# Kernel optimization log

Measured on AMD Instinct MI355X. Metric: run time of the kernel, lower is better.

## Reference

```python
import jax, jax.numpy as jnp
import numpy as np

C = 1024
T = 2048
B = 8

def setup_inputs() -> dict:
    key = jax.random.key(0)
    ks = jax.random.split(key, 7)
    s = lambda fan_in: 1.0 / np.sqrt(fan_in)
    return {
        "x":     jax.random.normal(ks[0], (B, T, C), dtype=jnp.float32),
        "w_qkv": jax.random.uniform(ks[1], (C, 3 * C), jnp.float32, -s(C), s(C)),
        "w_proj": jax.random.uniform(ks[2], (C, C), jnp.float32, -s(C), s(C)),
        "w1":    jax.random.uniform(ks[3], (C, 2 * C), jnp.float32, -s(C), s(C)),
        "w2":    jax.random.uniform(ks[4], (2 * C, C), jnp.float32, -s(2 * C), s(2 * C)),
        "g1":    jnp.ones((C,), jnp.float32),
        "g2":    jnp.ones((C,), jnp.float32),
    }

def rmsnorm(x, g, eps=1e-6):
    return x * jax.lax.rsqrt(jnp.mean(x * x, axis=-1, keepdims=True) + eps) * g

def reference(x, w_qkv, w_proj, w1, w2, g1, g2):
    t = x.shape[1]
    # --- attention ---
    h = rmsnorm(x, g1)
    qkv = h @ w_qkv                               # [B,T,3C]
    q, k, v = jnp.split(qkv, 3, axis=-1)
    scores = jnp.einsum('bqc,bkc->bqk', q, k) * (C ** -0.5)  # [B,T,T]
    causal = jnp.triu(jnp.ones((t, t), dtype=bool), k=1)
    scores = jnp.where(causal, -jnp.inf, scores)
    attn = jax.nn.softmax(scores, axis=-1)
    x = x + (attn @ v) @ w_proj
    # --- ffn ---
    h = rmsnorm(x, g2)
    return x + (jax.nn.silu(h @ w1)) @ w2
```

## Files before the change

### kernel.cpp

```cpp
#include <hip/hip_runtime.h>
#include <hip/hip_bf16.h>
#include <stdint.h>


#define C_DIM 1024
#define T_DIM 2048
#define B_DIM 8

typedef float f32x4 __attribute__((ext_vector_type(4)));
typedef __bf16 bf16x8 __attribute__((ext_vector_type(8)));

typedef const __attribute__((address_space(1))) void gvoid_t;
typedef __attribute__((address_space(3))) void lvoid_t;

__device__ __forceinline__ void gload_lds16(const void* g, void* l) {
    __builtin_amdgcn_global_load_lds((gvoid_t*)g, (lvoid_t*)l, 16, 0, 0);
}

__device__ __forceinline__ unsigned short f2bf_bits(float f) {
    __hip_bfloat16 h = __float2bfloat16(f);
    return *reinterpret_cast<unsigned short*>(&h);
}

__device__ __forceinline__ void xcd_remap(int& bx, int& by, int& bz) {
    const int gx = gridDim.x, gy = gridDim.y;
    const int nwg = gx * gy * (int)gridDim.z;
    const int orig = bx + gx * (by + gy * bz);
    const int q = nwg >> 3, r = nwg & 7;
    const int xcd = orig & 7, pos = orig >> 3;
    const int neu = (xcd < r ? xcd * (q + 1) : r * (q + 1) + (xcd - r) * q) + pos;
    bx = neu % gx;
    const int t = neu / gx;
    by = t % gy;
    bz = t / gy;
}

template<int EPI, int CMODE>
__global__ __launch_bounds__(256)
void gemm128(const __hip_bfloat16* A, const __hip_bfloat16* Bt,
             void* Cout, const void* Rv, void* C2, void* C3,
             int K, int lda, int ldb, int ldc,
             long long sA, long long sB, long long sC, float scale)
{
    int bx = blockIdx.x, by = blockIdx.y, bz = blockIdx.z;
    xcd_remap(bx, by, bz);
    if constexpr (CMODE == 1) { if (bx > by) return; }

    const int tid  = threadIdx.x;
    const int lane = tid & 63, wave = tid >> 6;
    const int l15  = lane & 15, l4 = lane >> 4;
    const int wr   = wave >> 1, wc = wave & 1;
    const int m0   = by * 128, n0 = bx * 128;

    A  += (long long)bz * sA;
    Bt += (long long)bz * sB;

    __shared__ __align__(16) char lds_[32768];

    int kmax = K;
    if constexpr (CMODE == 2) { int km = m0 + 128; kmax = km < K ? km : K; }
    const int NT = kmax >> 6;

    const int sr = lane >> 3;
    const int ss = (lane & 7) ^ sr;
    const __hip_bfloat16* Ag = A  + (long long)(m0 + 32 * wave + sr) * lda + ss * 8;
    const __hip_bfloat16* Bg = Bt + (long long)(n0 + 32 * wave + sr) * ldb + ss * 8;
    char* lAw = lds_ + wave * 4096;
    char* lBw = lds_ + 16384 + wave * 4096;

    const int offk0 = l15 * 128 + (((l4)     ^ (l15 & 7)) << 4);
    const int offk1 = l15 * 128 + (((4 + l4) ^ (l15 & 7)) << 4);

    f32x4 acc[4][4];
#pragma unroll
    for (int i = 0; i < 4; ++i)
#pragma unroll
        for (int j = 0; j < 4; ++j) acc[i][j] = (f32x4){0.f, 0.f, 0.f, 0.f};

    for (int t = 0; t < NT; ++t) {
#pragma unroll
        for (int i = 0; i < 4; ++i) {
            gload_lds16(Ag + (long long)t * 64 + i * 8 * lda, lAw + i * 1024);
            gload_lds16(Bg + (long long)t * 64 + i * 8 * ldb, lBw + i * 1024);
        }
        asm volatile("s_waitcnt vmcnt(0)" ::: "memory");
        __builtin_amdgcn_s_barrier();

        bf16x8 aR[4][2], bR[4][2];
#pragma unroll
        for (int mf = 0; mf < 4; ++mf) {
            const char* p = lds_ + (wr * 64 + mf * 16) * 128;
            aR[mf][0] = *(const bf16x8*)(p + offk0);
            aR[mf][1] = *(const bf16x8*)(p + offk1);
        }
#pragma unroll
        for (int nf = 0; nf < 4; ++nf) {
            const char* p = lds_ + 16384 + (wc * 64 + nf * 16) * 128;
            bR[nf][0] = *(const bf16x8*)(p + offk0);
            bR[nf][1] = *(const bf16x8*)(p + offk1);
        }
        __builtin_amdgcn_s_setprio(1);
#pragma unroll
        for (int mf = 0; mf < 4; ++mf)
#pragma unroll
            for (int nf = 0; nf < 4; ++nf)
#pragma unroll
                for (int ks = 0; ks < 2; ++ks)
                    acc[mf][nf] = __builtin_amdgcn_mfma_f32_16x16x32_bf16(
                        aR[mf][ks], bR[nf][ks], acc[mf][nf], 0, 0, 0);
        __builtin_amdgcn_s_setprio(0);
        asm volatile("s_waitcnt lgkmcnt(0)" ::: "memory");
        __builtin_amdgcn_s_barrier();
    }

    const long long cbase = (long long)bz * sC;
#pragma unroll
    for (int mf = 0; mf < 4; ++mf) {
        const int rbase = m0 + wr * 64 + mf * 16 + l4 * 4;
#pragma unroll
        for (int nf = 0; nf < 4; ++nf) {
            const int col = n0 + wc * 64 + nf * 16 + l15;
#pragma unroll
            for (int r = 0; r < 4; ++r) {
                const float v = acc[mf][nf][r];
                const int row = rbase + r;
                if constexpr (EPI == 6) {
                    const int seg = col >> 10, ncol = col & 1023;
                    if (seg == 0) {
                        ((__hip_bfloat16*)Cout)[(long long)row * 1024 + ncol] =
                            __float2bfloat16(v);
                    } else if (seg == 1) {
                        ((__hip_bfloat16*)C2)[(long long)row * 1024 + ncol] =
                            __float2bfloat16(v);
                    } else {
                        ((__hip_bfloat16*)C3)[((long long)(row >> 11) * C_DIM + ncol) * T_DIM
                                              + (row & 2047)] = __float2bfloat16(v);
                    }
                } else {
                    const long long idx = cbase + (long long)row * ldc + col;
                    if constexpr (EPI == 0) {
                        ((__hip_bfloat16*)Cout)[idx] = __float2bfloat16(v);
                    } else if constexpr (EPI == 3) {
                        const float s = v / (1.f + __expf(-v));
                        ((__hip_bfloat16*)Cout)[idx] = __float2bfloat16(s);
                    } else if constexpr (EPI == 4) {
                        ((__hip_bfloat16*)Cout)[idx] = __float2bfloat16(v * scale);
                    } else if constexpr (EPI == 8) {
                        const float xr = ((const float*)Rv)[idx];
                        ((__hip_bfloat16*)Cout)[idx] = __float2bfloat16(v + xr);
                    } else {
                        const float xr =
                            __bfloat162float(((const __hip_bfloat16*)Rv)[idx]);
                        ((float*)Cout)[idx] = v + xr;
                    }
                }
            }
        }
    }
}

template<bool BF16IN>
__global__ __launch_bounds__(256)
void rmsnorm_kernel(const void* __restrict__ xin, const float* __restrict__ g,
                    __hip_bfloat16* __restrict__ out)
{
    const long long row = blockIdx.x;
    const int tid = threadIdx.x;
    float e0, e1, e2, e3;
    if constexpr (BF16IN) {
        const ushort4 u = ((const ushort4*)((const __hip_bfloat16*)xin + row * C_DIM))[tid];
        e0 = __uint_as_float((unsigned)u.x << 16);
        e1 = __uint_as_float((unsigned)u.y << 16);
        e2 = __uint_as_float((unsigned)u.z << 16);
        e3 = __uint_as_float((unsigned)u.w << 16);
    } else {
        const float4 v = ((const float4*)((const float*)xin + row * C_DIM))[tid];
        e0 = v.x; e1 = v.y; e2 = v.z; e3 = v.w;
    }
    float ss = e0 * e0 + e1 * e1 + e2 * e2 + e3 * e3;
#pragma unroll
    for (int off = 32; off; off >>= 1) ss += __shfl_xor(ss, off);
    __shared__ float red[4];
    if ((tid & 63) == 0) red[tid >> 6] = ss;
    __syncthreads();
    ss = red[0] + red[1] + red[2] + red[3];
    const float sc = rsqrtf(ss * (1.0f / C_DIM) + 1e-6f);
    const float4 gv = ((const float4*)g)[tid];
    ushort4 u;
    u.x = f2bf_bits(e0 * sc * gv.x);
    u.y = f2bf_bits(e1 * sc * gv.y);
    u.z = f2bf_bits(e2 * sc * gv.z);
    u.w = f2bf_bits(e3 * sc * gv.w);
    *(ushort4*)(out + row * C_DIM + tid * 4) = u;
}

__global__ __launch_bounds__(256)
void softmax_causal(__hip_bfloat16* __restrict__ SP)
{
    const int i = blockIdx.x, b = blockIdx.y;
    __hip_bfloat16* row = SP + ((long long)b * T_DIM + i) * T_DIM;
    const int tid = threadIdx.x;
    const int jbase = tid * 8;

    uint4 raw = ((const uint4*)row)[tid];
    float v[8];
    const unsigned w[4] = {raw.x, raw.y, raw.z, raw.w};
#pragma unroll
    for (int c = 0; c < 4; ++c) {
        unsigned lo = w[c] << 16;
        unsigned hi = w[c] & 0xFFFF0000u;
        v[2 * c]     = __uint_as_float(lo);
        v[2 * c + 1] = __uint_as_float(hi);
    }
#pragma unroll
    for (int e = 0; e < 8; ++e)
        if (jbase + e > i) v[e] = -1e30f;

    float m = v[0];
#pragma unroll
    for (int e = 1; e < 8; ++e) m = fmaxf(m, v[e]);
#pragma unroll
    for (int off = 32; off; off >>= 1) m = fmaxf(m, __shfl_xor(m, off));
    __shared__ float redm[4], reds[4];
    if ((tid & 63) == 0) redm[tid >> 6] = m;
    __syncthreads();
    m = fmaxf(fmaxf(redm[0], redm[1]), fmaxf(redm[2], redm[3]));

    float e8[8];
    float s = 0.f;
#pragma unroll
    for (int e = 0; e < 8; ++e) { e8[e] = __expf(v[e] - m); s += e8[e]; }
#pragma unroll
    for (int off = 32; off; off >>= 1) s += __shfl_xor(s, off);
    if ((tid & 63) == 0) reds[tid >> 6] = s;
    __syncthreads();
    s = reds[0] + reds[1] + reds[2] + reds[3];
    const float inv = 1.f / s;

    uint4 outw;
    unsigned o[4];
#pragma unroll
    for (int c = 0; c < 4; ++c) {
        unsigned lo = f2bf_bits(e8[2 * c] * inv);
        unsigned hi = f2bf_bits(e8[2 * c + 1] * inv);
        o[c] = lo | (hi << 16);
    }
    outw.x = o[0]; outw.y = o[1]; outw.z = o[2]; outw.w = o[3];
    ((uint4*)row)[tid] = outw;
}

__global__ __launch_bounds__(256)
void wcast_t(const float* __restrict__ in, __hip_bfloat16* __restrict__ out,
             int K, int N)
{
    __shared__ float t[32][33];
    const int n0 = blockIdx.x * 32, k0 = blockIdx.y * 32;
    const int tx = threadIdx.x, ty = threadIdx.y;
#pragma unroll
    for (int r = ty; r < 32; r += 8)
        t[r][tx] = in[(long long)(k0 + r) * N + n0 + tx];
    __syncthreads();
#pragma unroll
    for (int r = ty; r < 32; r += 8)
        out[(long long)(n0 + r) * K + k0 + tx] = __float2bfloat16(t[tx][r]);
}

extern "C" void kernel_launch(void* const* d_in, const int* in_sizes, int n_in,
                              void* d_out, int out_size, void* d_ws, size_t ws_size,
                              hipStream_t stream)
{
    const float* x      = (const float*)d_in[0];
    const float* w_qkv  = (const float*)d_in[1];
    const float* w_proj = (const float*)d_in[2];
    const float* w1     = (const float*)d_in[3];
    const float* w2     = (const float*)d_in[4];
    const float* g1     = (const float*)d_in[5];
    const float* g2     = (const float*)d_in[6];
    float* out = (float*)d_out;
    char* ws = (char*)d_ws;

    const size_t SP_off = 0;
    const size_t h_off  = 0;
    const size_t u_off  = 0;
    const size_t q_off  = 67108864ull;
    const size_t k_off  = 100663296ull;
    const size_t vT_off = 134217728ull;
    const size_t wq_off = 167772160ull;
    const size_t wp_off = wq_off + 6291456ull;
    const size_t w1_off = wp_off + 2097152ull;
    const size_t w2_off = w1_off + 4194304ull;
    const size_t NEED   = w2_off + 4194304ull;

    if (ws_size < NEED) return;

    auto bf = [&](size_t off) { return (__hip_bfloat16*)(ws + off); };

    wcast_t<<<dim3(96, 32), dim3(32, 8), 0, stream>>>(w_qkv,  bf(wq_off), 1024, 3072);
    wcast_t<<<dim3(32, 32), dim3(32, 8), 0, stream>>>(w_proj, bf(wp_off), 1024, 1024);
    wcast_t<<<dim3(64, 32), dim3(32, 8), 0, stream>>>(w1,     bf(w1_off), 1024, 2048);
    wcast_t<<<dim3(32, 64), dim3(32, 8), 0, stream>>>(w2,     bf(w2_off), 2048, 1024);

    rmsnorm_kernel<false><<<16384, 256, 0, stream>>>(x, g1, bf(h_off));

    gemm128<6, 0><<<dim3(24, 128, 1), 256, 0, stream>>>(
        bf(h_off), bf(wq_off), bf(q_off), nullptr, bf(k_off), bf(vT_off),
        1024, 1024, 1024, 1024, 0, 0, 0, 1.f);

    gemm128<4, 1><<<dim3(16, 16, 8), 256, 0, stream>>>(
        bf(q_off), bf(k_off), bf(SP_off), nullptr, nullptr, nullptr,
        1024, 1024, 1024, 2048,
        (long long)T_DIM * C_DIM, (long long)T_DIM * C_DIM, (long long)T_DIM * T_DIM,
        0.03125f);

    softmax_causal<<<dim3(2048, 8), 256, 0, stream>>>(bf(SP_off));

    gemm128<0, 2><<<dim3(8, 16, 8), 256, 0, stream>>>(
        bf(SP_off), bf(vT_off), bf(k_off) , nullptr, nullptr, nullptr,
        2048, 2048, 2048, 1024,
        (long long)T_DIM * T_DIM, (long long)C_DIM * T_DIM, (long long)T_DIM * C_DIM,
        1.f);

    gemm128<8, 0><<<dim3(8, 128, 1), 256, 0, stream>>>(
        bf(k_off) , bf(wp_off), bf(vT_off) , x, nullptr, nullptr,
        1024, 1024, 1024, 1024, 0, 0, 0, 1.f);

    rmsnorm_kernel<true><<<16384, 256, 0, stream>>>(bf(vT_off), g2, bf(q_off));

    gemm128<3, 0><<<dim3(16, 128, 1), 256, 0, stream>>>(
        bf(q_off), bf(w1_off), bf(u_off), nullptr, nullptr, nullptr,
        1024, 1024, 1024, 2048, 0, 0, 0, 1.f);

    gemm128<9, 0><<<dim3(8, 128, 1), 256, 0, stream>>>(
        bf(u_off), bf(w2_off), out, bf(vT_off) , nullptr, nullptr,
        2048, 2048, 2048, 1024, 0, 0, 0, 1.f);
}
```

Measured before the change: 573.9 us.

## Triple-buffer GEMM K-loop with templated tiles and skip masked softmax blocks

The GEMM kernel becomes a template over wave grid and per-wave tile counts. It now uses a three-stage LDS ring with K-step 32, so global-to-LDS loads for tiles t+2 overlap MFMA work on tile t. The dense projection and FFN GEMMs move to 256x256 tiles with 512 threads, which gives more reuse per load but fewer blocks and more register pressure. Softmax now skips loading and storing the causally masked columns beyond each row's 128-block boundary, cutting memory traffic on the score matrix.

```diff
diff --git a/kernel.cpp b/kernel.cpp
--- a/kernel.cpp
+++ b/kernel.cpp
@@ -35,13 +35,19 @@
     bz = t / gy;
 }
 
-template<int EPI, int CMODE>
-__global__ __launch_bounds__(256)
-void gemm128(const __hip_bfloat16* A, const __hip_bfloat16* Bt,
-             void* Cout, const void* Rv, void* C2, void* C3,
-             int K, int lda, int ldb, int ldc,
-             long long sA, long long sB, long long sC, float scale)
-{
+template<int EPI, int CMODE, int WM, int WN, int TM, int TN>
+__global__ __launch_bounds__(WM*WN*64, (WM*WN > 4) ? 2 : 3)
+void gemmk(const __hip_bfloat16* A, const __hip_bfloat16* Bt,
+           void* Cout, const void* Rv, void* C2, void* C3,
+           int K, int lda, int ldb, int ldc,
+           long long sA, long long sB, long long sC, float scale)
+{
+    constexpr int NW = WM * WN;
+    constexpr int BM = WM * TM * 16, BN = WN * TN * 16;
+    constexpr int ABYTES = BM * 64, BBYTES = BN * 64;
+    constexpr int TILEB = ABYTES + BBYTES;
+    constexpr int IA = BM / (16 * NW), IB = BN / (16 * NW);
+
     int bx = blockIdx.x, by = blockIdx.y, bz = blockIdx.z;
     xcd_remap(bx, by, bz);
     if constexpr (CMODE == 1) { if (bx > by) return; }
@@ -49,77 +55,94 @@
     const int tid  = threadIdx.x;
     const int lane = tid & 63, wave = tid >> 6;
     const int l15  = lane & 15, l4 = lane >> 4;
-    const int wr   = wave >> 1, wc = wave & 1;
-    const int m0   = by * 128, n0 = bx * 128;
+    const int wm   = wave / WN, wn = wave % WN;
+    const int m0   = by * BM, n0 = bx * BN;
 
     A  += (long long)bz * sA;
     Bt += (long long)bz * sB;
 
-    __shared__ __align__(16) char lds_[32768];
+    __shared__ __align__(16) char lds_[3 * TILEB];
 
     int kmax = K;
-    if constexpr (CMODE == 2) { int km = m0 + 128; kmax = km < K ? km : K; }
-    const int NT = kmax >> 6;
-
-    const int sr = lane >> 3;
-    const int ss = (lane & 7) ^ sr;
-    const __hip_bfloat16* Ag = A  + (long long)(m0 + 32 * wave + sr) * lda + ss * 8;
-    const __hip_bfloat16* Bg = Bt + (long long)(n0 + 32 * wave + sr) * ldb + ss * 8;
-    char* lAw = lds_ + wave * 4096;
-    char* lBw = lds_ + 16384 + wave * 4096;
-
-    const int offk0 = l15 * 128 + (((l4)     ^ (l15 & 7)) << 4);
-    const int offk1 = l15 * 128 + (((4 + l4) ^ (l15 & 7)) << 4);
-
-    f32x4 acc[4][4];
-#pragma unroll
-    for (int i = 0; i < 4; ++i)
-#pragma unroll
-        for (int j = 0; j < 4; ++j) acc[i][j] = (f32x4){0.f, 0.f, 0.f, 0.f};
+    if constexpr (CMODE == 2) { int km = m0 + BM; kmax = km < K ? km : K; }
+    const int NT = kmax >> 5;
+
+    const __hip_bfloat16* AgP[IA];
+    const __hip_bfloat16* BgP[IB];
+#pragma unroll
+    for (int i = 0; i < IA; ++i) {
+        const int g = (i * NW + wave) * 64 + lane;
+        const int row = g >> 2, c = (g & 3) ^ (row & 3);
+        AgP[i] = A + (long long)(m0 + row) * lda + c * 8;
+    }
+#pragma unroll
+    for (int i = 0; i < IB; ++i) {
+        const int g = (i * NW + wave) * 64 + lane;
+        const int row = g >> 2, c = (g & 3) ^ (row & 3);
+        BgP[i] = Bt + (long long)(n0 + row) * ldb + c * 8;
+    }
+
+    auto stage = [&](int sb, int t) {
+        char* base = lds_ + sb * TILEB;
+#pragma unroll
+        for (int i = 0; i < IA; ++i)
+            gload_lds16(AgP[i] + t * 32, base + (i * NW + wave) * 1024);
+#pragma unroll
+        for (int i = 0; i < IB; ++i)
+            gload_lds16(BgP[i] + t * 32, base + ABYTES + (i * NW + wave) * 1024);
+    };
+
+    const int roff = l15 * 64 + ((l4 ^ (l15 & 3)) << 4);
+    const int aw = wm * TM * 1024;
+    const int bw = wn * TN * 1024;
+
+    f32x4 acc[TM][TN];
+#pragma unroll
+    for (int i = 0; i < TM; ++i)
+#pragma unroll
+        for (int j = 0; j < TN; ++j) acc[i][j] = (f32x4){0.f, 0.f, 0.f, 0.f};
+
+    stage(0, 0);
+    stage(1, 1);
+    asm volatile("s_waitcnt vmcnt(4)" ::: "memory");
+    asm volatile("s_barrier" ::: "memory");
 
     for (int t = 0; t < NT; ++t) {
-#pragma unroll
-        for (int i = 0; i < 4; ++i) {
-            gload_lds16(Ag + (long long)t * 64 + i * 8 * lda, lAw + i * 1024);
-            gload_lds16(Bg + (long long)t * 64 + i * 8 * ldb, lBw + i * 1024);
-        }
-        asm volatile("s_waitcnt vmcnt(0)" ::: "memory");
-        __builtin_amdgcn_s_barrier();
-
-        bf16x8 aR[4][2], bR[4][2];
-#pragma unroll
-        for (int mf = 0; mf < 4; ++mf) {
-            const char* p = lds_ + (wr * 64 + mf * 16) * 128;
-            aR[mf][0] = *(const bf16x8*)(p + offk0);
-            aR[mf][1] = *(const bf16x8*)(p + offk1);
-        }
-#pragma unroll
-        for (int nf = 0; nf < 4; ++nf) {
-            const char* p = lds_ + 16384 + (wc * 64 + nf * 16) * 128;
-            bR[nf][0] = *(const bf16x8*)(p + offk0);
-            bR[nf][1] = *(const bf16x8*)(p + offk1);
-        }
+        const int buf = t % 3;
+        const bool stg = (t + 2) < NT;
+        if (stg) stage((t + 2) % 3, t + 2);
+
+        const char* ab = lds_ + buf * TILEB;
+        const char* bb = ab + ABYTES;
+        bf16x8 aR[TM], bR[TN];
+#pragma unroll
+        for (int mf = 0; mf < TM; ++mf)
+            aR[mf] = *(const bf16x8*)(ab + aw + mf * 1024 + roff);
+#pragma unroll
+        for (int nf = 0; nf < TN; ++nf)
+            bR[nf] = *(const bf16x8*)(bb + bw + nf * 1024 + roff);
+
         __builtin_amdgcn_s_setprio(1);
 #pragma unroll
-        for (int mf = 0; mf < 4; ++mf)
-#pragma unroll
-            for (int nf = 0; nf < 4; ++nf)
-#pragma unroll
-                for (int ks = 0; ks < 2; ++ks)
-                    acc[mf][nf] = __builtin_amdgcn_mfma_f32_16x16x32_bf16(
-                        aR[mf][ks], bR[nf][ks], acc[mf][nf], 0, 0, 0);
+        for (int mf = 0; mf < TM; ++mf)
+#pragma unroll
+            for (int nf = 0; nf < TN; ++nf)
+                acc[mf][nf] = __builtin_amdgcn_mfma_f32_16x16x32_bf16(
+                    aR[mf], bR[nf], acc[mf][nf], 0, 0, 0);
         __builtin_amdgcn_s_setprio(0);
-        asm volatile("s_waitcnt lgkmcnt(0)" ::: "memory");
-        __builtin_amdgcn_s_barrier();
+
+        if (stg) asm volatile("s_waitcnt vmcnt(4)" ::: "memory");
+        else     asm volatile("s_waitcnt vmcnt(0)" ::: "memory");
+        asm volatile("s_barrier" ::: "memory");
     }
 
     const long long cbase = (long long)bz * sC;
 #pragma unroll
-    for (int mf = 0; mf < 4; ++mf) {
-        const int rbase = m0 + wr * 64 + mf * 16 + l4 * 4;
-#pragma unroll
-        for (int nf = 0; nf < 4; ++nf) {
-            const int col = n0 + wc * 64 + nf * 16 + l15;
+    for (int mf = 0; mf < TM; ++mf) {
+        const int rbase = m0 + wm * TM * 16 + mf * 16 + l4 * 4;
+#pragma unroll
+        for (int nf = 0; nf < TN; ++nf) {
+            const int col = n0 + wn * TN * 16 + nf * 16 + l15;
 #pragma unroll
             for (int r = 0; r < 4; ++r) {
                 const float v = acc[mf][nf][r];
@@ -201,20 +224,25 @@
     __hip_bfloat16* row = SP + ((long long)b * T_DIM + i) * T_DIM;
     const int tid = threadIdx.x;
     const int jbase = tid * 8;
-
-    uint4 raw = ((const uint4*)row)[tid];
+    const int kmax = ((i >> 7) + 1) << 7;
+    const bool act = jbase < kmax;
+
     float v[8];
-    const unsigned w[4] = {raw.x, raw.y, raw.z, raw.w};
-#pragma unroll
-    for (int c = 0; c < 4; ++c) {
-        unsigned lo = w[c] << 16;
-        unsigned hi = w[c] & 0xFFFF0000u;
-        v[2 * c]     = __uint_as_float(lo);
-        v[2 * c + 1] = __uint_as_float(hi);
-    }
-#pragma unroll
-    for (int e = 0; e < 8; ++e)
-        if (jbase + e > i) v[e] = -1e30f;
+    if (act) {
+        uint4 raw = ((const uint4*)row)[tid];
+        const unsigned w[4] = {raw.x, raw.y, raw.z, raw.w};
+#pragma unroll
+        for (int c = 0; c < 4; ++c) {
+            v[2 * c]     = __uint_as_float(w[c] << 16);
+            v[2 * c + 1] = __uint_as_float(w[c] & 0xFFFF0000u);
+        }
+#pragma unroll
+        for (int e = 0; e < 8; ++e)
+            if (jbase + e > i) v[e] = -1e30f;
+    } else {
+#pragma unroll
+        for (int e = 0; e < 8; ++e) v[e] = -1e30f;
+    }
 
     float m = v[0];
 #pragma unroll
@@ -237,16 +265,18 @@
     s = reds[0] + reds[1] + reds[2] + reds[3];
     const float inv = 1.f / s;
 
-    uint4 outw;
-    unsigned o[4];
-#pragma unroll
-    for (int c = 0; c < 4; ++c) {
-        unsigned lo = f2bf_bits(e8[2 * c] * inv);
-        unsigned hi = f2bf_bits(e8[2 * c + 1] * inv);
-        o[c] = lo | (hi << 16);
-    }
-    outw.x = o[0]; outw.y = o[1]; outw.z = o[2]; outw.w = o[3];
-    ((uint4*)row)[tid] = outw;
+    if (act) {
+        uint4 outw;
+        unsigned o[4];
+#pragma unroll
+        for (int c = 0; c < 4; ++c) {
+            unsigned lo = f2bf_bits(e8[2 * c] * inv);
+            unsigned hi = f2bf_bits(e8[2 * c + 1] * inv);
+            o[c] = lo | (hi << 16);
+        }
+        outw.x = o[0]; outw.y = o[1]; outw.z = o[2]; outw.w = o[3];
+        ((uint4*)row)[tid] = outw;
+    }
 }
 
 __global__ __launch_bounds__(256)
@@ -302,11 +332,11 @@
 
     rmsnorm_kernel<false><<<16384, 256, 0, stream>>>(x, g1, bf(h_off));
 
-    gemm128<6, 0><<<dim3(24, 128, 1), 256, 0, stream>>>(
+    gemmk<6, 0, 2, 4, 8, 4><<<dim3(12, 64, 1), 512, 0, stream>>>(
         bf(h_off), bf(wq_off), bf(q_off), nullptr, bf(k_off), bf(vT_off),
         1024, 1024, 1024, 1024, 0, 0, 0, 1.f);
 
-    gemm128<4, 1><<<dim3(16, 16, 8), 256, 0, stream>>>(
+    gemmk<4, 1, 2, 2, 4, 4><<<dim3(16, 16, 8), 256, 0, stream>>>(
         bf(q_off), bf(k_off), bf(SP_off), nullptr, nullptr, nullptr,
         1024, 1024, 1024, 2048,
         (long long)T_DIM * C_DIM, (long long)T_DIM * C_DIM, (long long)T_DIM * T_DIM,
@@ -314,23 +344,23 @@
 
     softmax_causal<<<dim3(2048, 8), 256, 0, stream>>>(bf(SP_off));
 
-    gemm128<0, 2><<<dim3(8, 16, 8), 256, 0, stream>>>(
+    gemmk<0, 2, 2, 2, 4, 4><<<dim3(8, 16, 8), 256, 0, stream>>>(
         bf(SP_off), bf(vT_off), bf(k_off) , nullptr, nullptr, nullptr,
         2048, 2048, 2048, 1024,
         (long long)T_DIM * T_DIM, (long long)C_DIM * T_DIM, (long long)T_DIM * C_DIM,
         1.f);
 
-    gemm128<8, 0><<<dim3(8, 128, 1), 256, 0, stream>>>(
+    gemmk<8, 0, 2, 4, 8, 4><<<dim3(4, 64, 1), 512, 0, stream>>>(
         bf(k_off) , bf(wp_off), bf(vT_off) , x, nullptr, nullptr,
         1024, 1024, 1024, 1024, 0, 0, 0, 1.f);
 
     rmsnorm_kernel<true><<<16384, 256, 0, stream>>>(bf(vT_off), g2, bf(q_off));
 
-    gemm128<3, 0><<<dim3(16, 128, 1), 256, 0, stream>>>(
+    gemmk<3, 0, 2, 4, 8, 4><<<dim3(8, 64, 1), 512, 0, stream>>>(
         bf(q_off), bf(w1_off), bf(u_off), nullptr, nullptr, nullptr,
         1024, 1024, 1024, 2048, 0, 0, 0, 1.f);
 
-    gemm128<9, 0><<<dim3(8, 128, 1), 256, 0, stream>>>(
+    gemmk<9, 0, 2, 4, 8, 4><<<dim3(4, 64, 1), 512, 0, stream>>>(
         bf(u_off), bf(w2_off), out, bf(vT_off) , nullptr, nullptr,
         2048, 2048, 2048, 1024, 0, 0, 0, 1.f);
 }
```

After: 586.5 us. +2.2%, slower.

## Double-buffer GEMM tiles, split QKV projection, skip masked softmax chunks

Applied to the files above, without the earlier changes.

Adds a dense GEMM kernel that prefetches the next 64-wide K tile into a second LDS buffer while computing on the current one. It hides global-load latency behind MFMA work, using 64KB of LDS and a launch-bounds occupancy hint. The attention GEMMs move to a separate double-buffered kernel with a 32-wide K step. The fused QKV projection becomes three launches, and the causal softmax skips loading and storing chunks beyond each row's 128-column block. The trade-offs are more launches and lower occupancy from the larger LDS footprint.

```diff
diff --git a/kernel.cpp b/kernel.cpp
--- a/kernel.cpp
+++ b/kernel.cpp
@@ -35,16 +35,14 @@
     bz = t / gy;
 }
 
-template<int EPI, int CMODE>
-__global__ __launch_bounds__(256)
-void gemm128(const __hip_bfloat16* A, const __hip_bfloat16* Bt,
-             void* Cout, const void* Rv, void* C2, void* C3,
-             int K, int lda, int ldb, int ldc,
-             long long sA, long long sB, long long sC, float scale)
+template<int EPI>
+__global__ __launch_bounds__(256, 2)
+void gemm128d(const __hip_bfloat16* A, const __hip_bfloat16* Bt,
+              void* Cout, const void* Rv,
+              int K, int lda, int ldb, int ldc)
 {
     int bx = blockIdx.x, by = blockIdx.y, bz = blockIdx.z;
     xcd_remap(bx, by, bz);
-    if constexpr (CMODE == 1) { if (bx > by) return; }
 
     const int tid  = threadIdx.x;
     const int lane = tid & 63, wave = tid >> 6;
@@ -52,21 +50,15 @@
     const int wr   = wave >> 1, wc = wave & 1;
     const int m0   = by * 128, n0 = bx * 128;
 
-    A  += (long long)bz * sA;
-    Bt += (long long)bz * sB;
-
-    __shared__ __align__(16) char lds_[32768];
-
-    int kmax = K;
-    if constexpr (CMODE == 2) { int km = m0 + 128; kmax = km < K ? km : K; }
-    const int NT = kmax >> 6;
-
-    const int sr = lane >> 3;
-    const int ss = (lane & 7) ^ sr;
-    const __hip_bfloat16* Ag = A  + (long long)(m0 + 32 * wave + sr) * lda + ss * 8;
-    const __hip_bfloat16* Bg = Bt + (long long)(n0 + 32 * wave + sr) * ldb + ss * 8;
-    char* lAw = lds_ + wave * 4096;
-    char* lBw = lds_ + 16384 + wave * 4096;
+    __shared__ __align__(16) char lds_[65536];
+
+    const int NT = K >> 6;
+
+    const int srow = tid >> 3;
+    const int schk = (tid & 7) ^ (srow & 7);
+    const __hip_bfloat16* Ag = A + (long long)(m0 + srow) * lda + schk * 8;
+    const __hip_bfloat16* Bg = Bt + (long long)(n0 + srow) * ldb + schk * 8;
+    char* ldsw = lds_ + (wave * 64) * 16;
 
     const int offk0 = l15 * 128 + (((l4)     ^ (l15 & 7)) << 4);
     const int offk1 = l15 * 128 + (((4 + l4) ^ (l15 & 7)) << 4);
@@ -77,25 +69,37 @@
 #pragma unroll
         for (int j = 0; j < 4; ++j) acc[i][j] = (f32x4){0.f, 0.f, 0.f, 0.f};
 
+    auto stage = [&](int buf, int t) {
+        char* ab = ldsw + buf * 32768;
+        char* bb = ab + 16384;
+        const long long koff = (long long)t * 64;
+#pragma unroll
+        for (int i = 0; i < 4; ++i) {
+            gload_lds16(Ag + koff + (long long)i * 32 * lda, ab + i * 4096);
+            gload_lds16(Bg + koff + (long long)i * 32 * ldb, bb + i * 4096);
+        }
+    };
+
+    stage(0, 0);
+    asm volatile("s_waitcnt vmcnt(0)" ::: "memory");
+    __builtin_amdgcn_s_barrier();
+
     for (int t = 0; t < NT; ++t) {
-#pragma unroll
-        for (int i = 0; i < 4; ++i) {
-            gload_lds16(Ag + (long long)t * 64 + i * 8 * lda, lAw + i * 1024);
-            gload_lds16(Bg + (long long)t * 64 + i * 8 * ldb, lBw + i * 1024);
-        }
-        asm volatile("s_waitcnt vmcnt(0)" ::: "memory");
-        __builtin_amdgcn_s_barrier();
-
+        const int buf = t & 1;
+        if (t + 1 < NT) stage(buf ^ 1, t + 1);
+
+        const char* ab = lds_ + buf * 32768;
+        const char* bb = ab + 16384;
         bf16x8 aR[4][2], bR[4][2];
 #pragma unroll
         for (int mf = 0; mf < 4; ++mf) {
-            const char* p = lds_ + (wr * 64 + mf * 16) * 128;
+            const char* p = ab + (wr * 64 + mf * 16) * 128;
             aR[mf][0] = *(const bf16x8*)(p + offk0);
             aR[mf][1] = *(const bf16x8*)(p + offk1);
         }
 #pragma unroll
         for (int nf = 0; nf < 4; ++nf) {
-            const char* p = lds_ + 16384 + (wc * 64 + nf * 16) * 128;
+            const char* p = bb + (wc * 64 + nf * 16) * 128;
             bR[nf][0] = *(const bf16x8*)(p + offk0);
             bR[nf][1] = *(const bf16x8*)(p + offk1);
         }
@@ -109,11 +113,12 @@
                     acc[mf][nf] = __builtin_amdgcn_mfma_f32_16x16x32_bf16(
                         aR[mf][ks], bR[nf][ks], acc[mf][nf], 0, 0, 0);
         __builtin_amdgcn_s_setprio(0);
+
         asm volatile("s_waitcnt lgkmcnt(0)" ::: "memory");
+        asm volatile("s_waitcnt vmcnt(0)" ::: "memory");
         __builtin_amdgcn_s_barrier();
     }
 
-    const long long cbase = (long long)bz * sC;
 #pragma unroll
     for (int mf = 0; mf < 4; ++mf) {
         const int rbase = m0 + wr * 64 + mf * 16 + l4 * 4;
@@ -124,27 +129,16 @@
             for (int r = 0; r < 4; ++r) {
                 const float v = acc[mf][nf][r];
                 const int row = rbase + r;
-                if constexpr (EPI == 6) {
-                    const int seg = col >> 10, ncol = col & 1023;
-                    if (seg == 0) {
-                        ((__hip_bfloat16*)Cout)[(long long)row * 1024 + ncol] =
-                            __float2bfloat16(v);
-                    } else if (seg == 1) {
-                        ((__hip_bfloat16*)C2)[(long long)row * 1024 + ncol] =
-                            __float2bfloat16(v);
-                    } else {
-                        ((__hip_bfloat16*)C3)[((long long)(row >> 11) * C_DIM + ncol) * T_DIM
-                                              + (row & 2047)] = __float2bfloat16(v);
-                    }
+                if constexpr (EPI == 5) {
+                    ((__hip_bfloat16*)Cout)[((long long)(row >> 11) * C_DIM + col) * T_DIM
+                                            + (row & 2047)] = __float2bfloat16(v);
                 } else {
-                    const long long idx = cbase + (long long)row * ldc + col;
+                    const long long idx = (long long)row * ldc + col;
                     if constexpr (EPI == 0) {
                         ((__hip_bfloat16*)Cout)[idx] = __float2bfloat16(v);
                     } else if constexpr (EPI == 3) {
                         const float s = v / (1.f + __expf(-v));
                         ((__hip_bfloat16*)Cout)[idx] = __float2bfloat16(s);
-                    } else if constexpr (EPI == 4) {
-                        ((__hip_bfloat16*)Cout)[idx] = __float2bfloat16(v * scale);
                     } else if constexpr (EPI == 8) {
                         const float xr = ((const float*)Rv)[idx];
                         ((__hip_bfloat16*)Cout)[idx] = __float2bfloat16(v + xr);
@@ -153,6 +147,109 @@
                             __bfloat162float(((const __hip_bfloat16*)Rv)[idx]);
                         ((float*)Cout)[idx] = v + xr;
                     }
+                }
+            }
+        }
+    }
+}
+
+template<int EPI, int CMODE>
+__global__ __launch_bounds__(256)
+void gemm128(const __hip_bfloat16* A, const __hip_bfloat16* Bt,
+             void* Cout, int K, int lda, int ldb, int ldc,
+             long long sA, long long sB, long long sC, float scale)
+{
+    int bx = blockIdx.x, by = blockIdx.y, bz = blockIdx.z;
+    xcd_remap(bx, by, bz);
+    if constexpr (CMODE == 1) { if (bx > by) return; }
+
+    const int tid  = threadIdx.x;
+    const int lane = tid & 63, wave = tid >> 6;
+    const int l15  = lane & 15, l4 = lane >> 4;
+    const int wr   = wave >> 1, wc = wave & 1;
+    const int m0   = by * 128, n0 = bx * 128;
+    const int z    = bz;
+
+    A  += (long long)z * sA;
+    Bt += (long long)z * sB;
+
+    __shared__ __align__(16) short As[2][128 * 32];
+    __shared__ __align__(16) short Bs[2][128 * 32];
+
+    int kmax = K;
+    if constexpr (CMODE == 2) { int km = m0 + 128; kmax = km < K ? km : K; }
+
+    f32x4 acc[4][4];
+#pragma unroll
+    for (int i = 0; i < 4; ++i)
+#pragma unroll
+        for (int j = 0; j < 4; ++j) acc[i][j] = (f32x4){0.f, 0.f, 0.f, 0.f};
+
+    const int srow  = wave * 32 + (lane >> 2);
+    const int sbyte = (((lane & 3) ^ ((lane >> 2) & 3))) << 4;
+    const char* Ag = (const char*)(A  + (long long)(m0 + srow) * lda) + sbyte;
+    const char* Bg = (const char*)(Bt + (long long)(n0 + srow) * ldb) + sbyte;
+    const long long astep = (long long)16 * lda * 2;
+    const long long bstep = (long long)16 * ldb * 2;
+    char* AsW[2] = {(char*)As[0] + wave * 2048, (char*)As[1] + wave * 2048};
+    char* BsW[2] = {(char*)Bs[0] + wave * 2048, (char*)Bs[1] + wave * 2048};
+
+    auto stage = [&](int buf, int k0) {
+        const char* ag = Ag + (long long)k0 * 2;
+        const char* bg = Bg + (long long)k0 * 2;
+        gload_lds16(ag,         AsW[buf]);
+        gload_lds16(ag + astep, AsW[buf] + 1024);
+        gload_lds16(bg,         BsW[buf]);
+        gload_lds16(bg + bstep, BsW[buf] + 1024);
+    };
+
+    const int cs16 = ((l4 ^ (l15 & 3)) << 4);
+
+    stage(0, 0);
+    __syncthreads();
+
+    for (int k0 = 0; k0 < kmax; k0 += 32) {
+        const int buf = (k0 >> 5) & 1;
+        if (k0 + 32 < kmax) stage(buf ^ 1, k0 + 32);
+
+        const char* Ac = (const char*)As[buf];
+        const char* Bc = (const char*)Bs[buf];
+        bf16x8 af[4], bfr[4];
+#pragma unroll
+        for (int mi = 0; mi < 4; ++mi) {
+            int row = wr * 64 + mi * 16 + l15;
+            af[mi] = *(const bf16x8*)(Ac + row * 64 + cs16);
+        }
+#pragma unroll
+        for (int ni = 0; ni < 4; ++ni) {
+            int col = wc * 64 + ni * 16 + l15;
+            bfr[ni] = *(const bf16x8*)(Bc + col * 64 + cs16);
+        }
+#pragma unroll
+        for (int mi = 0; mi < 4; ++mi)
+#pragma unroll
+            for (int ni = 0; ni < 4; ++ni)
+                acc[mi][ni] = __builtin_amdgcn_mfma_f32_16x16x32_bf16(
+                    af[mi], bfr[ni], acc[mi][ni], 0, 0, 0);
+
+        __syncthreads();
+    }
+
+    const long long cbase = (long long)z * sC;
+#pragma unroll
+    for (int mi = 0; mi < 4; ++mi) {
+        const int rbase = m0 + wr * 64 + mi * 16 + l4 * 4;
+#pragma unroll
+        for (int ni = 0; ni < 4; ++ni) {
+            const int col = n0 + wc * 64 + ni * 16 + l15;
+#pragma unroll
+            for (int r = 0; r < 4; ++r) {
+                const long long idx = cbase + (long long)(rbase + r) * ldc + col;
+                const float v = acc[mi][ni][r];
+                if constexpr (EPI == 0) {
+                    ((__hip_bfloat16*)Cout)[idx] = __float2bfloat16(v);
+                } else {
+                    ((__hip_bfloat16*)Cout)[idx] = __float2bfloat16(v * scale);
                 }
             }
         }
@@ -201,20 +298,25 @@
     __hip_bfloat16* row = SP + ((long long)b * T_DIM + i) * T_DIM;
     const int tid = threadIdx.x;
     const int jbase = tid * 8;
-
-    uint4 raw = ((const uint4*)row)[tid];
+    const int kmax = ((i >> 7) + 1) << 7;
+    const bool act = jbase < kmax;
+
     float v[8];
-    const unsigned w[4] = {raw.x, raw.y, raw.z, raw.w};
-#pragma unroll
-    for (int c = 0; c < 4; ++c) {
-        unsigned lo = w[c] << 16;
-        unsigned hi = w[c] & 0xFFFF0000u;
-        v[2 * c]     = __uint_as_float(lo);
-        v[2 * c + 1] = __uint_as_float(hi);
-    }
-#pragma unroll
-    for (int e = 0; e < 8; ++e)
-        if (jbase + e > i) v[e] = -1e30f;
+    if (act) {
+        uint4 raw = ((const uint4*)row)[tid];
+        const unsigned w[4] = {raw.x, raw.y, raw.z, raw.w};
+#pragma unroll
+        for (int c = 0; c < 4; ++c) {
+            v[2 * c]     = __uint_as_float(w[c] << 16);
+            v[2 * c + 1] = __uint_as_float(w[c] & 0xFFFF0000u);
+        }
+#pragma unroll
+        for (int e = 0; e < 8; ++e)
+            if (jbase + e > i) v[e] = -1e30f;
+    } else {
+#pragma unroll
+        for (int e = 0; e < 8; ++e) v[e] = -1e30f;
+    }
 
     float m = v[0];
 #pragma unroll
@@ -237,16 +339,18 @@
     s = reds[0] + reds[1] + reds[2] + reds[3];
     const float inv = 1.f / s;
 
-    uint4 outw;
-    unsigned o[4];
-#pragma unroll
-    for (int c = 0; c < 4; ++c) {
-        unsigned lo = f2bf_bits(e8[2 * c] * inv);
-        unsigned hi = f2bf_bits(e8[2 * c + 1] * inv);
-        o[c] = lo | (hi << 16);
-    }
-    outw.x = o[0]; outw.y = o[1]; outw.z = o[2]; outw.w = o[3];
-    ((uint4*)row)[tid] = outw;
+    if (act) {
+        uint4 outw;
+        unsigned o[4];
+#pragma unroll
+        for (int c = 0; c < 4; ++c) {
+            unsigned lo = f2bf_bits(e8[2 * c] * inv);
+            unsigned hi = f2bf_bits(e8[2 * c + 1] * inv);
+            o[c] = lo | (hi << 16);
+        }
+        outw.x = o[0]; outw.y = o[1]; outw.z = o[2]; outw.w = o[3];
+        ((uint4*)row)[tid] = outw;
+    }
 }
 
 __global__ __launch_bounds__(256)
@@ -302,12 +406,17 @@
 
     rmsnorm_kernel<false><<<16384, 256, 0, stream>>>(x, g1, bf(h_off));
 
-    gemm128<6, 0><<<dim3(24, 128, 1), 256, 0, stream>>>(
-        bf(h_off), bf(wq_off), bf(q_off), nullptr, bf(k_off), bf(vT_off),
-        1024, 1024, 1024, 1024, 0, 0, 0, 1.f);
+    gemm128d<0><<<dim3(8, 128, 1), 256, 0, stream>>>(
+        bf(h_off), bf(wq_off), bf(q_off), nullptr, 1024, 1024, 1024, 1024);
+    gemm128d<0><<<dim3(8, 128, 1), 256, 0, stream>>>(
+        bf(h_off), bf(wq_off) + 1024 * 1024, bf(k_off), nullptr,
+        1024, 1024, 1024, 1024);
+    gemm128d<5><<<dim3(8, 128, 1), 256, 0, stream>>>(
+        bf(h_off), bf(wq_off) + 2 * 1024 * 1024, bf(vT_off), nullptr,
+        1024, 1024, 1024, 2048);
 
     gemm128<4, 1><<<dim3(16, 16, 8), 256, 0, stream>>>(
-        bf(q_off), bf(k_off), bf(SP_off), nullptr, nullptr, nullptr,
+        bf(q_off), bf(k_off), bf(SP_off),
         1024, 1024, 1024, 2048,
         (long long)T_DIM * C_DIM, (long long)T_DIM * C_DIM, (long long)T_DIM * T_DIM,
         0.03125f);
@@ -315,22 +424,22 @@
     softmax_causal<<<dim3(2048, 8), 256, 0, stream>>>(bf(SP_off));
 
     gemm128<0, 2><<<dim3(8, 16, 8), 256, 0, stream>>>(
-        bf(SP_off), bf(vT_off), bf(k_off) , nullptr, nullptr, nullptr,
+        bf(SP_off), bf(vT_off), bf(k_off) ,
         2048, 2048, 2048, 1024,
         (long long)T_DIM * T_DIM, (long long)C_DIM * T_DIM, (long long)T_DIM * C_DIM,
         1.f);
 
-    gemm128<8, 0><<<dim3(8, 128, 1), 256, 0, stream>>>(
-        bf(k_off) , bf(wp_off), bf(vT_off) , x, nullptr, nullptr,
-        1024, 1024, 1024, 1024, 0, 0, 0, 1.f);
+    gemm128d<8><<<dim3(8, 128, 1), 256, 0, stream>>>(
+        bf(k_off) , bf(wp_off), bf(vT_off) , x,
+        1024, 1024, 1024, 1024);
 
     rmsnorm_kernel<true><<<16384, 256, 0, stream>>>(bf(vT_off), g2, bf(q_off));
 
-    gemm128<3, 0><<<dim3(16, 128, 1), 256, 0, stream>>>(
-        bf(q_off), bf(w1_off), bf(u_off), nullptr, nullptr, nullptr,
-        1024, 1024, 1024, 2048, 0, 0, 0, 1.f);
-
-    gemm128<9, 0><<<dim3(8, 128, 1), 256, 0, stream>>>(
-        bf(u_off), bf(w2_off), out, bf(vT_off) , nullptr, nullptr,
-        2048, 2048, 2048, 1024, 0, 0, 0, 1.f);
-}
+    gemm128d<3><<<dim3(16, 128, 1), 256, 0, stream>>>(
+        bf(q_off), bf(w1_off), bf(u_off), nullptr,
+        1024, 1024, 1024, 2048);
+
+    gemm128d<9><<<dim3(8, 128, 1), 256, 0, stream>>>(
+        bf(u_off), bf(w2_off), out, bf(vT_off) ,
+        2048, 2048, 2048, 1024);
+}
```

Result: faster. 531.6 us (-7.4%).
